# Kernel optimization log

Measured on AMD Instinct MI355X. Metric: run time of the kernel, lower is better.

Reference implementation:

```python
import jax, jax.numpy as jnp
import numpy as np

B, S, H, I, E, K = 2, 1024, 768, 1536, 8, 2
CAPACITY_FACTOR = 1.5
ROUTING_TEMP = 1.0
LB_WEIGHT = 0.001


def setup_inputs() -> dict:
    key = jax.random.key(0)
    k_x, k_g, k_w1, k_w3, k_w2 = jax.random.split(key, 5)
    std = 0.02
    return {
        "x": jax.random.normal(k_x, (B, S, H), dtype=jnp.float32),
        "w_gate": jax.random.normal(k_g, (H, E), dtype=jnp.float32) * 0.02,
        "w1": jax.random.normal(k_w1, (E, H, I), dtype=jnp.float32) * std,
        "w3": jax.random.normal(k_w3, (E, H, I), dtype=jnp.float32) * std,
        "w2": jax.random.normal(k_w2, (E, I, H), dtype=jnp.float32) * (std / np.sqrt(2 * 12)),
    }


def _moe_forward(x, w_gate, w1, w3, w2):
    Bb, Ss, Hh = x.shape
    T = Bb * Ss
    xf = x.reshape(T, Hh)

    # --- routing ---
    gate_logits = (xf @ w_gate) / ROUTING_TEMP          # [T, E]
    gate_probs = jax.nn.softmax(gate_logits, axis=-1)   # [T, E]
    topk_probs, topk_idx = jax.lax.top_k(gate_probs, K)  # [T, K]
    topk_probs = topk_probs / (topk_probs.sum(-1, keepdims=True) + 1e-8)

    # --- capacity dropping (per-k slot, token order, like the torch loop) ---
    capacity = max(8, int((T * K // E) * CAPACITY_FACTOR))
    onehot = (topk_idx[:, :, None] == jnp.arange(E)[None, None, :])  # [T, K, E] bool
    ranks = jnp.cumsum(onehot.astype(jnp.int32), axis=0)             # position of token in expert queue
    keep = onehot & (ranks <= capacity)                               # [T, K, E]

    # combine weight per (token, expert): sum over k of kept, clamped routing prob
    w_clamped = jnp.clip(topk_probs, 1e-8, 10.0)                      # [T, K]
    combine = jnp.einsum("tk,tke->te", w_clamped, keep.astype(xf.dtype))  # [T, E]

    # --- dense per-expert SwiGLU (reference form of masked dispatch) ---
    g = jnp.einsum("th,ehi->tei", xf, w1)   # [T, E, I]
    u = jnp.einsum("th,ehi->tei", xf, w3)   # [T, E, I]
    h = jax.nn.silu(g) * u                    # [T, E, I]
    y = jnp.einsum("tei,eih->teh", h, w2)   # [T, E, H]
    out = jnp.einsum("te,teh->th", combine, y).reshape(Bb, Ss, Hh)

    # --- load balancing loss ---
    expert_counts = keep.sum(axis=(0, 1)).astype(jnp.float32)         # [E]
    dropped = (onehot.sum() - keep.sum()).astype(jnp.float32)
    expert_usage = jax.lax.stop_gradient(expert_counts) / float(max(T * K, 1))
    gate_importance = gate_probs.mean(axis=0)                          # [E]
    aux = jnp.sum(expert_usage * gate_importance) * E
    aux = aux + jnp.where(dropped > 0, dropped / float(max(T, 1)) * 0.1, 0.0)
    aux = jnp.minimum(aux, 1.0) * LB_WEIGHT
    return out, aux


def reference(x, w_gate, w1, w3, w2):
    return _moe_forward(x, w_gate, w1, w3, w2)
```

## Files before the change

kernel.cpp:

```cpp
#include <hip/hip_runtime.h>
#include <math.h>

#define T_TOK 2048
#define HD 768
#define ID 1536
#define NE 8
#define CAP 768
#define TK 4096
#define RT 12
#define NB1 24
#define KC1 24
#define NB2 12
#define KC2 48

typedef __bf16 bf16_t;
typedef __bf16 bf16x8 __attribute__((ext_vector_type(8)));
typedef __bf16 bf16x4 __attribute__((ext_vector_type(4)));
typedef float floatx4 __attribute__((ext_vector_type(4)));

__device__ __forceinline__ void gld16(const bf16_t* g, bf16_t* l) {
  __builtin_amdgcn_global_load_lds(
      (__attribute__((address_space(1))) void*)(g),
      (__attribute__((address_space(3))) void*)(l),
      16, 0, 0);
}

__global__ void k_prep(const float* __restrict__ x, const float* __restrict__ wg,
                       const float* __restrict__ w1, const float* __restrict__ w3,
                       const float* __restrict__ w2,
                       bf16_t* __restrict__ xbf, bf16_t* __restrict__ w1b,
                       bf16_t* __restrict__ w3b, bf16_t* __restrict__ w2b,
                       int2* __restrict__ idx2, float2* __restrict__ wc2,
                       float* __restrict__ probs8, float* __restrict__ outz) {
  int b = blockIdx.x;
  int tid = threadIdx.x;
  if (b < 512) {
#pragma unroll
    for (int k2 = 0; k2 < 3; ++k2) {
      float4 z = make_float4(0.f, 0.f, 0.f, 0.f);
      *(float4*)(outz + (size_t)b * 3072 + k2 * 1024 + tid * 4) = z;
    }
    int t = b * 4 + (tid >> 6);
    int lane = tid & 63;
    const float* xr = x + (size_t)t * HD;
    int off = lane * 12;
    float4 a = *(const float4*)(xr + off);
    float4 bv = *(const float4*)(xr + off + 4);
    float4 c = *(const float4*)(xr + off + 8);
    float xv[12] = {a.x, a.y, a.z, a.w, bv.x, bv.y, bv.z, bv.w, c.x, c.y, c.z, c.w};
    bf16x4 s0, s1, s2;
#pragma unroll
    for (int j = 0; j < 4; ++j) { s0[j] = (bf16_t)xv[j]; s1[j] = (bf16_t)xv[4 + j]; s2[j] = (bf16_t)xv[8 + j]; }
    bf16_t* xo = xbf + (size_t)t * HD + off;
    *(bf16x4*)xo = s0; *(bf16x4*)(xo + 4) = s1; *(bf16x4*)(xo + 8) = s2;

    float acc[8] = {0, 0, 0, 0, 0, 0, 0, 0};
#pragma unroll
    for (int jj = 0; jj < 12; ++jj) {
      const float4* wr = (const float4*)(wg + (size_t)(off + jj) * 8);
      float4 w0 = wr[0], w1v = wr[1];
      float v = xv[jj];
      acc[0] += v * w0.x; acc[1] += v * w0.y; acc[2] += v * w0.z; acc[3] += v * w0.w;
      acc[4] += v * w1v.x; acc[5] += v * w1v.y; acc[6] += v * w1v.z; acc[7] += v * w1v.w;
    }
#pragma unroll
    for (int e = 0; e < 8; ++e) {
      float v = acc[e];
      for (int s = 1; s < 64; s <<= 1) v += __shfl_xor(v, s, 64);
      acc[e] = v;
    }
    float mx = acc[0];
#pragma unroll
    for (int e = 1; e < 8; ++e) mx = fmaxf(mx, acc[e]);
    float p[8], sum = 0.f;
#pragma unroll
    for (int e = 0; e < 8; ++e) { p[e] = __expf(acc[e] - mx); sum += p[e]; }
#pragma unroll
    for (int e = 0; e < 8; ++e) p[e] /= sum;
    if (lane == 0) {
      float4 P0 = make_float4(p[0], p[1], p[2], p[3]);
      float4 P1 = make_float4(p[4], p[5], p[6], p[7]);
      *(float4*)&probs8[t * 8] = P0;
      *(float4*)&probs8[t * 8 + 4] = P1;
      int e0 = 0;
#pragma unroll
      for (int e = 1; e < 8; ++e) if (p[e] > p[e0]) e0 = e;
      int e1 = (e0 == 0) ? 1 : 0;
#pragma unroll
      for (int e = 0; e < 8; ++e) if (e != e0 && p[e] > p[e1]) e1 = e;
      float denom = p[e0] + p[e1] + 1e-8f;
      float w0c = fminf(fmaxf(p[e0] / denom, 1e-8f), 10.f);
      float w1c = fminf(fmaxf(p[e1] / denom, 1e-8f), 10.f);
      idx2[t] = make_int2(e0, e1);
      wc2[t] = make_float2(w0c, w1c);
    }
  } else {
    __shared__ bf16_t sm[32 * 68];
    int ib = b - 512;
    const float* src; bf16_t* dst; int C, KC;
    if (ib < 192) {
      int e = ib & 7, nb = ib >> 3;
      src = w1 + (size_t)e * HD * ID + nb * 64;
      dst = w1b + (size_t)((e * NB1 + nb) * KC1) * 2048;
      C = ID; KC = KC1;
    } else if (ib < 384) {
      int e = (ib - 192) & 7, nb = (ib - 192) >> 3;
      src = w3 + (size_t)e * HD * ID + nb * 64;
      dst = w3b + (size_t)((e * NB1 + nb) * KC1) * 2048;
      C = ID; KC = KC1;
    } else {
      int e = (ib - 384) & 7, nb = (ib - 384) >> 3;
      src = w2 + (size_t)e * ID * HD + nb * 64;
      dst = w2b + (size_t)((e * NB2 + nb) * KC2) * 2048;
      C = HD; KC = KC2;
    }
    int r = tid >> 3, t7 = tid & 7;
    int n = tid >> 2, pch = tid & 3;
    int cl = pch ^ ((n >> 1) & 3);
    for (int kc = 0; kc < KC; ++kc) {
      const float* sp = src + (size_t)(kc * 32 + r) * C + t7 * 8;
      float4 va = *(const float4*)sp;
      float4 vb = *(const float4*)(sp + 4);
      bf16x4 ba, bb;
      ba[0] = (bf16_t)va.x; ba[1] = (bf16_t)va.y; ba[2] = (bf16_t)va.z; ba[3] = (bf16_t)va.w;
      bb[0] = (bf16_t)vb.x; bb[1] = (bf16_t)vb.y; bb[2] = (bf16_t)vb.z; bb[3] = (bf16_t)vb.w;
      *(bf16x4*)&sm[r * 68 + t7 * 8] = ba;
      *(bf16x4*)&sm[r * 68 + t7 * 8 + 4] = bb;
      __syncthreads();
      bf16x8 o;
#pragma unroll
      for (int j = 0; j < 8; ++j) o[j] = sm[(cl * 8 + j) * 68 + n];
      *(bf16x8*)(dst + (size_t)kc * 2048 + tid * 8) = o;
      __syncthreads();
    }
  }
}

__global__ void k_scan(const int2* __restrict__ idx2, const float2* __restrict__ wc2,
                       const float* __restrict__ probs8,
                       int* __restrict__ tok_of_row, float* __restrict__ wgt_of_row,
                       int2* __restrict__ cnt_start, float* __restrict__ aux_out) {
  __shared__ int2 sIdx[2048];
  __shared__ float2 sWc[2048];
  __shared__ int sTot[16];
  __shared__ int sPos[8];
  __shared__ float sImp[16][8];
  int tid = threadIdx.x;
  sIdx[tid] = idx2[tid]; sIdx[tid + 1024] = idx2[tid + 1024];
  sWc[tid] = wc2[tid];  sWc[tid + 1024] = wc2[tid + 1024];
  const float4* pp = (const float4*)probs8;
  float4 u0 = pp[tid * 4], u1 = pp[tid * 4 + 1], u2 = pp[tid * 4 + 2], u3 = pp[tid * 4 + 3];
  float im[8] = {u0.x + u2.x, u0.y + u2.y, u0.z + u2.z, u0.w + u2.w,
                 u1.x + u3.x, u1.y + u3.y, u1.z + u3.z, u1.w + u3.w};
#pragma unroll
  for (int e = 0; e < 8; ++e) {
    float v = im[e];
    for (int d = 1; d < 64; d <<= 1) v += __shfl_xor(v, d, 64);
    im[e] = v;
  }
  int w = tid >> 6, lane = tid & 63;
  if (lane == 0) {
#pragma unroll
    for (int e = 0; e < 8; ++e) sImp[w][e] = im[e];
  }
  __syncthreads();
  int s = w >> 3, e = w & 7;
  int t0 = lane * 32;
  int cnt = 0;
  for (int j = 0; j < 32; ++j) {
    int2 p = sIdx[t0 + j];
    cnt += ((s ? p.y : p.x) == e) ? 1 : 0;
  }
  int incl = cnt;
  for (int d = 1; d < 64; d <<= 1) {
    int v = __shfl_up(incl, d, 64);
    if (lane >= d) incl += v;
  }
  int excl = incl - cnt;
  if (lane == 63) sTot[w] = incl;
  __syncthreads();
  if (tid == 0) {
    int run = 0; float a = 0.f;
    for (int ee = 0; ee < 8; ++ee) {
      float impv = 0.f;
      for (int ww = 0; ww < 16; ++ww) impv += sImp[ww][ee];
      int k = min(sTot[ee], CAP) + min(sTot[8 + ee], CAP);
      sPos[ee] = run;
      cnt_start[ee] = make_int2(run, k);
      a += ((float)k / (float)TK) * (impv / (float)T_TOK);
      run += k;
    }
    a *= (float)NE;
    int dropped = TK - run;
    if (dropped > 0) a += (float)dropped / (float)T_TOK * 0.1f;
    aux_out[0] = fminf(a, 1.f) * 0.001f;
  }
  __syncthreads();
  int rank = excl;
  for (int j = 0; j < 32; ++j) {
    int t = t0 + j;
    int2 p = sIdx[t];
    int ex = s ? p.y : p.x;
    if (ex == e) {
      rank++;
      if (rank <= CAP) {
        int pos = atomicAdd(&sPos[e], 1);
        tok_of_row[pos] = t;
        float2 wv = sWc[t];
        wgt_of_row[pos] = s ? wv.y : wv.x;
      }
    }
  }
}

__global__ __launch_bounds__(256, 4)
void k_gemm1(const bf16_t* __restrict__ xbf, const bf16_t* __restrict__ w1b,
             const bf16_t* __restrict__ w3b, const int* __restrict__ tok_of_row,
             const int2* __restrict__ cnt_start, bf16_t* __restrict__ h_ws) {
  int e = blockIdx.x & 7;
  int t = blockIdx.x >> 3;
  int nb = t / RT, rt = t - nb * RT;
  int2 cs = cnt_start[e];
  int nrows = cs.y - rt * 128;
  if (nrows <= 0) return;
  if (nrows > 128) nrows = 128;
  int grow0 = cs.x + rt * 128;

  __shared__ __attribute__((aligned(16))) bf16_t Abuf[128 * 32];
  __shared__ __attribute__((aligned(16))) bf16_t B1buf[64 * 32];
  __shared__ __attribute__((aligned(16))) bf16_t B3buf[64 * 32];

  int tid = threadIdx.x;
  int lane = tid & 63, wv = tid >> 6;
  int wm = wv & 1, wn = wv >> 1;
  int lr = lane & 15, q = lane >> 4;
  int rdc = (q ^ ((lane >> 1) & 3)) * 8;
  int srow = lane >> 2;
  int gch = ((lane & 3) ^ ((lane >> 3) & 3)) * 8;

  int ra = wv * 32 + srow;
  int tokA0 = tok_of_row[grow0 + min(ra, nrows - 1)];
  int tokA1 = tok_of_row[grow0 + min(ra + 16, nrows - 1)];
  const bf16_t* gA0 = xbf + (size_t)tokA0 * HD + gch;
  const bf16_t* gA1 = xbf + (size_t)tokA1 * HD + gch;
  const bf16_t* p1 = w1b + (size_t)((e * NB1 + nb) * KC1) * 2048 + tid * 8;
  const bf16_t* p3 = w3b + (size_t)((e * NB1 + nb) * KC1) * 2048 + tid * 8;
  bf16_t* lA0 = &Abuf[(wv * 32) * 32];
  bf16_t* lA1 = &Abuf[(wv * 32 + 16) * 32];
  bf16_t* lB1 = &B1buf[wv * 512];
  bf16_t* lB3 = &B3buf[wv * 512];

  floatx4 accg[4][2] = {};
  floatx4 accu[4][2] = {};

  for (int kk = 0; kk < KC1; ++kk) {
    __syncthreads();
    gld16(gA0, lA0); gld16(gA1, lA1);
    gld16(p1, lB1); gld16(p3, lB3);
    gA0 += 32; gA1 += 32; p1 += 2048; p3 += 2048;
    __syncthreads();
    bf16x8 af[4], b1f[2], b3f[2];
#pragma unroll
    for (int i = 0; i < 4; ++i) af[i] = *(const bf16x8*)&Abuf[(wm * 64 + i * 16 + lr) * 32 + rdc];
#pragma unroll
    for (int i = 0; i < 2; ++i) b1f[i] = *(const bf16x8*)&B1buf[(wn * 32 + i * 16 + lr) * 32 + rdc];
#pragma unroll
    for (int i = 0; i < 2; ++i) b3f[i] = *(const bf16x8*)&B3buf[(wn * 32 + i * 16 + lr) * 32 + rdc];
#pragma unroll
    for (int i = 0; i < 4; ++i)
#pragma unroll
      for (int jj = 0; jj < 2; ++jj) {
        accg[i][jj] = __builtin_amdgcn_mfma_f32_16x16x32_bf16(af[i], b1f[jj], accg[i][jj], 0, 0, 0);
        accu[i][jj] = __builtin_amdgcn_mfma_f32_16x16x32_bf16(af[i], b3f[jj], accu[i][jj], 0, 0, 0);
      }
  }
#pragma unroll
  for (int i = 0; i < 4; ++i)
#pragma unroll
    for (int r = 0; r < 4; ++r) {
      int rl = wm * 64 + i * 16 + q * 4 + r;
      if (rl < nrows) {
        size_t rb = (size_t)(grow0 + rl) * ID + nb * 64 + wn * 32 + lr;
#pragma unroll
        for (int jj = 0; jj < 2; ++jj) {
          float gg = accg[i][jj][r], uu = accu[i][jj][r];
          float sg = gg / (1.f + __expf(-gg));
          h_ws[rb + jj * 16] = (bf16_t)(sg * uu);
        }
      }
    }
}

__global__ __launch_bounds__(256, 4)
void k_gemm2(const bf16_t* __restrict__ h_ws, const bf16_t* __restrict__ w2b,
             const int* __restrict__ tok_of_row, const float* __restrict__ wgt_of_row,
             const int2* __restrict__ cnt_start, float* __restrict__ out) {
  int e = blockIdx.x & 7;
  int t = blockIdx.x >> 3;
  int nb = t / RT, rt = t - nb * RT;
  int2 cs = cnt_start[e];
  int nrows = cs.y - rt * 128;
  if (nrows <= 0) return;
  if (nrows > 128) nrows = 128;
  int grow0 = cs.x + rt * 128;

  __shared__ __attribute__((aligned(16))) bf16_t Abuf[128 * 32];
  __shared__ __attribute__((aligned(16))) bf16_t Bbuf[64 * 32];

  int tid = threadIdx.x;
  int lane = tid & 63, wv = tid >> 6;
  int wm = wv & 1, wn = wv >> 1;
  int lr = lane & 15, q = lane >> 4;
  int rdc = (q ^ ((lane >> 1) & 3)) * 8;
  int srow = lane >> 2;
  int gch = ((lane & 3) ^ ((lane >> 3) & 3)) * 8;

  int ra = wv * 32 + srow;
  const bf16_t* gA0 = h_ws + (size_t)(grow0 + min(ra, nrows - 1)) * ID + gch;
  const bf16_t* gA1 = h_ws + (size_t)(grow0 + min(ra + 16, nrows - 1)) * ID + gch;
  const bf16_t* pB = w2b + (size_t)((e * NB2 + nb) * KC2) * 2048 + tid * 8;
  bf16_t* lA0 = &Abuf[(wv * 32) * 32];
  bf16_t* lA1 = &Abuf[(wv * 32 + 16) * 32];
  bf16_t* lB = &Bbuf[wv * 512];

  floatx4 acc[4][2] = {};

  for (int kk = 0; kk < KC2; ++kk) {
    __syncthreads();
    gld16(gA0, lA0); gld16(gA1, lA1);
    gld16(pB, lB);
    gA0 += 32; gA1 += 32; pB += 2048;
    __syncthreads();
    bf16x8 af[4], bfr[2];
#pragma unroll
    for (int i = 0; i < 4; ++i) af[i] = *(const bf16x8*)&Abuf[(wm * 64 + i * 16 + lr) * 32 + rdc];
#pragma unroll
    for (int i = 0; i < 2; ++i) bfr[i] = *(const bf16x8*)&Bbuf[(wn * 32 + i * 16 + lr) * 32 + rdc];
#pragma unroll
    for (int i = 0; i < 4; ++i)
#pragma unroll
      for (int jj = 0; jj < 2; ++jj)
        acc[i][jj] = __builtin_amdgcn_mfma_f32_16x16x32_bf16(af[i], bfr[jj], acc[i][jj], 0, 0, 0);
  }
#pragma unroll
  for (int i = 0; i < 4; ++i)
#pragma unroll
    for (int r = 0; r < 4; ++r) {
      int rl = wm * 64 + i * 16 + q * 4 + r;
      if (rl < nrows) {
        int grow = grow0 + rl;
        int tok = tok_of_row[grow];
        float wgt = wgt_of_row[grow];
        size_t ob = (size_t)tok * HD + nb * 64 + wn * 32 + lr;
#pragma unroll
        for (int jj = 0; jj < 2; ++jj)
          atomicAdd(&out[ob + jj * 16], wgt * acc[i][jj][r]);
      }
    }
}

extern "C" void kernel_launch(void* const* d_in, const int* in_sizes, int n_in,
                              void* d_out, int out_size, void* d_ws, size_t ws_size,
                              hipStream_t stream) {
  const float* x  = (const float*)d_in[0];
  const float* wg = (const float*)d_in[1];
  const float* w1 = (const float*)d_in[2];
  const float* w3 = (const float*)d_in[3];
  const float* w2 = (const float*)d_in[4];
  float* out = (float*)d_out;

  char* ws = (char*)d_ws;
  bf16_t* xbf  = (bf16_t*)(ws + 0);
  bf16_t* w1b  = (bf16_t*)(ws + 3145728);
  bf16_t* w3b  = (bf16_t*)(ws + 22020096);
  bf16_t* w2b  = (bf16_t*)(ws + 40894464);
  bf16_t* h_ws = (bf16_t*)(ws + 59768832);
  float*  probs8     = (float*)(ws + 72351744);
  int2*   idx2       = (int2*)(ws + 72417280);
  float2* wc2        = (float2*)(ws + 72433664);
  int*    tok_of_row = (int*)(ws + 72450048);
  float*  wgt_of_row = (float*)(ws + 72466432);
  int2*   cnt_start  = (int2*)(ws + 72482816);

  float* aux_out = out + (size_t)T_TOK * HD;

  k_prep<<<992, 256, 0, stream>>>(x, wg, w1, w3, w2, xbf, w1b, w3b, w2b,
                                  idx2, wc2, probs8, out);
  k_scan<<<1, 1024, 0, stream>>>(idx2, wc2, probs8, tok_of_row, wgt_of_row,
                                 cnt_start, aux_out);
  k_gemm1<<<8 * NB1 * RT, 256, 0, stream>>>(xbf, w1b, w3b, tok_of_row,
                                            cnt_start, h_ws);
  k_gemm2<<<8 * NB2 * RT, 256, 0, stream>>>(h_ws, w2b, tok_of_row, wgt_of_row,
                                            cnt_start, out);
}
```

Measured before the change: 277.8 us.

## Split weight-conversion panels across more blocks and drop the LDS transpose

The fp32-to-bf16 weight repacking in the prep kernel now splits each panel into 8-chunk pieces, so the grid grows from 992 to 2240 blocks. Each thread now reads its eight values straight from global memory with strided loads instead of staging through shared memory with two barriers per chunk. This aims to raise parallelism and remove synchronisation from a bandwidth-bound conversion step. The cost is uncoalesced column-strided global reads, which may waste memory bandwidth.

Result: faster. 262.2 us (-5.6%).

```diff
diff --git a/kernel.cpp b/kernel.cpp
--- a/kernel.cpp
+++ b/kernel.cpp
@@ -95,43 +95,40 @@
       wc2[t] = make_float2(w0c, w1c);
     }
   } else {
-    __shared__ bf16_t sm[32 * 68];
-    int ib = b - 512;
-    const float* src; bf16_t* dst; int C, KC;
-    if (ib < 192) {
-      int e = ib & 7, nb = ib >> 3;
-      src = w1 + (size_t)e * HD * ID + nb * 64;
-      dst = w1b + (size_t)((e * NB1 + nb) * KC1) * 2048;
-      C = ID; KC = KC1;
-    } else if (ib < 384) {
-      int e = (ib - 192) & 7, nb = (ib - 192) >> 3;
-      src = w3 + (size_t)e * HD * ID + nb * 64;
-      dst = w3b + (size_t)((e * NB1 + nb) * KC1) * 2048;
-      C = ID; KC = KC1;
+    int rb = b - 512;
+    const float* src; bf16_t* dst; int C; int kc0;
+    if (rb < 1152) {
+      int m = rb >= 576;
+      int r3 = m ? rb - 576 : rb;
+      int pan = r3 / 3;
+      kc0 = (r3 - pan * 3) * 8;
+      int e = pan & 7, nb = pan >> 3;
+      src = (m ? w3 : w1) + (size_t)e * HD * ID + nb * 64;
+      dst = (m ? w3b : w1b) + (size_t)(e * NB1 + nb) * (KC1 * 2048);
+      C = ID;
     } else {
-      int e = (ib - 384) & 7, nb = (ib - 384) >> 3;
+      int q = rb - 1152;
+      int pan = q / 6;
+      kc0 = (q - pan * 6) * 8;
+      int e = pan & 7, nb = pan >> 3;
       src = w2 + (size_t)e * ID * HD + nb * 64;
-      dst = w2b + (size_t)((e * NB2 + nb) * KC2) * 2048;
-      C = HD; KC = KC2;
-    }
-    int r = tid >> 3, t7 = tid & 7;
-    int n = tid >> 2, pch = tid & 3;
-    int cl = pch ^ ((n >> 1) & 3);
-    for (int kc = 0; kc < KC; ++kc) {
-      const float* sp = src + (size_t)(kc * 32 + r) * C + t7 * 8;
-      float4 va = *(const float4*)sp;
-      float4 vb = *(const float4*)(sp + 4);
-      bf16x4 ba, bb;
-      ba[0] = (bf16_t)va.x; ba[1] = (bf16_t)va.y; ba[2] = (bf16_t)va.z; ba[3] = (bf16_t)va.w;
-      bb[0] = (bf16_t)vb.x; bb[1] = (bf16_t)vb.y; bb[2] = (bf16_t)vb.z; bb[3] = (bf16_t)vb.w;
-      *(bf16x4*)&sm[r * 68 + t7 * 8] = ba;
-      *(bf16x4*)&sm[r * 68 + t7 * 8 + 4] = bb;
-      __syncthreads();
+      dst = w2b + (size_t)(e * NB2 + nb) * (KC2 * 2048);
+      C = HD;
+    }
+    int n = tid >> 2, p4 = tid & 3;
+    int c8 = p4 ^ ((n >> 1) & 3);
+    const float* sp0 = src + n + (size_t)(kc0 * 32 + c8 * 8) * C;
+    bf16_t* dp = dst + (size_t)kc0 * 2048 + tid * 8;
+#pragma unroll 2
+    for (int t = 0; t < 8; ++t) {
+      const float* sp = sp0 + (size_t)t * 32 * C;
+      float v[8];
+#pragma unroll
+      for (int j = 0; j < 8; ++j) v[j] = sp[(size_t)j * C];
       bf16x8 o;
 #pragma unroll
-      for (int j = 0; j < 8; ++j) o[j] = sm[(cl * 8 + j) * 68 + n];
-      *(bf16x8*)(dst + (size_t)kc * 2048 + tid * 8) = o;
-      __syncthreads();
+      for (int j = 0; j < 8; ++j) o[j] = (bf16_t)v[j];
+      *(bf16x8*)(dp + t * 2048) = o;
     }
   }
 }
@@ -384,8 +381,8 @@
 
   float* aux_out = out + (size_t)T_TOK * HD;
 
-  k_prep<<<992, 256, 0, stream>>>(x, wg, w1, w3, w2, xbf, w1b, w3b, w2b,
-                                  idx2, wc2, probs8, out);
+  k_prep<<<2240, 256, 0, stream>>>(x, wg, w1, w3, w2, xbf, w1b, w3b, w2b,
+                                   idx2, wc2, probs8, out);
   k_scan<<<1, 1024, 0, stream>>>(idx2, wc2, probs8, tok_of_row, wgt_of_row,
                                  cnt_start, aux_out);
   k_gemm1<<<8 * NB1 * RT, 256, 0, stream>>>(xbf, w1b, w3b, tok_of_row,
```
